# Performance work log

Measured on AMD Instinct MI355X. Metric: run time of the kernel, lower is better.

## Reference

```python
import jax, jax.numpy as jnp
import numpy as np

B, S, D, H = 4, 2048, 512, 8
DH = D // H  # head dim = 64
NEG = -1000000.0


def setup_inputs() -> dict:
    key = jax.random.key(0)
    ks = jax.random.split(key, 13)
    s = 1.0 / np.sqrt(D)
    return {
        "Q": jax.random.normal(ks[0], (B, S, D), jnp.float32),
        "K": jax.random.normal(ks[1], (B, S, D), jnp.float32),
        "V": jax.random.normal(ks[2], (B, S, D), jnp.float32),
        "Wq": jax.random.normal(ks[3], (D, D), jnp.float32) * s,
        "bq": jnp.zeros((D,), jnp.float32),
        "Wk": jax.random.normal(ks[4], (D, D), jnp.float32) * s,
        "bk": jnp.zeros((D,), jnp.float32),
        "Wv": jax.random.normal(ks[5], (D, D), jnp.float32) * s,
        "bv": jnp.zeros((D,), jnp.float32),
        "Wo": jax.random.normal(ks[6], (D, D), jnp.float32) * s,
        "bo": jnp.zeros((D,), jnp.float32),
        "masked": jax.random.randint(ks[7], (B,), 1, S + 1, jnp.int64),
    }


def _heads(x):
    # [B,S,D] -> [B,H,S,DH]
    return x.reshape(B, S, H, DH).transpose(0, 2, 1, 3)


def reference(Q, K, V, Wq, bq, Wk, bk, Wv, bv, Wo, bo, masked):
    q = _heads(Q @ Wq.T + bq)
    k = _heads(K @ Wk.T + bk)
    v = _heads(V @ Wv.T + bv)
    scores = jnp.einsum("bhqd,bhkd->bhqk", q, k) / jnp.sqrt(jnp.asarray(DH, q.dtype))
    # valid-length key mask, per batch (same for every head and query row)
    key_mask = jnp.arange(S)[None, None, None, :] < masked[:, None, None, None]
    scores = jnp.where(key_mask, scores, jnp.asarray(NEG, scores.dtype))
    weights = jax.nn.softmax(scores, axis=-1)
    out = jnp.einsum("bhqk,bhkd->bhqd", weights, v)  # [B,H,S,DH]
    out = out.transpose(0, 2, 1, 3).reshape(B, S, D)
    return out @ Wo.T + bo
```

## Files before the change

kernel.cpp:

```cpp
#include <hip/hip_runtime.h>
#include <stdint.h>


typedef __attribute__((ext_vector_type(8))) short short8;
typedef __attribute__((ext_vector_type(4))) float f32x4;
typedef __attribute__((ext_vector_type(4))) unsigned short u16x4;

#define MFMA16(a, b, c) __builtin_amdgcn_mfma_f32_16x16x32_bf16(a, b, c, 0, 0, 0)

#define SCALE_LOG2 0.18033688011112042f
#define FIXED_M    32.0f
#define MASKED_E2  -200.0f

__device__ __forceinline__ unsigned short f2bf(float f) {
    unsigned int x = __float_as_uint(f);
    unsigned int r = (x + 0x7fffu + ((x >> 16) & 1u)) >> 16;
    return (unsigned short)r;
}
__device__ __forceinline__ short8 load8(const unsigned short* p) {
    return *reinterpret_cast<const short8*>(p);
}
__device__ __forceinline__ void gload_lds16(const unsigned short* g, unsigned short* l) {
    __builtin_amdgcn_global_load_lds(
        (const __attribute__((address_space(1))) unsigned int*)g,
        (__attribute__((address_space(3))) unsigned int*)l, 16, 0, 0);
}

__global__ __launch_bounds__(256)
void convert_bf16(const float4* __restrict__ Q, const float4* __restrict__ K,
                  const float4* __restrict__ V, const float4* __restrict__ Wq,
                  const float4* __restrict__ Wk, const float4* __restrict__ Wv,
                  const float4* __restrict__ Wo, u16x4* __restrict__ dst)
{
    const int n = 3407872;
    for (int i = blockIdx.x * 256 + threadIdx.x; i < n; i += gridDim.x * 256) {
        const float4* src; int off;
        if      (i < 1048576) { src = Q;  off = i; }
        else if (i < 2097152) { src = K;  off = i - 1048576; }
        else if (i < 3145728) { src = V;  off = i - 2097152; }
        else if (i < 3211264) { src = Wq; off = i - 3145728; }
        else if (i < 3276800) { src = Wk; off = i - 3211264; }
        else if (i < 3342336) { src = Wv; off = i - 3276800; }
        else                  { src = Wo; off = i - 3342336; }
        const float4 v = src[off];
        u16x4 r;
        r[0] = f2bf(v.x); r[1] = f2bf(v.y); r[2] = f2bf(v.z); r[3] = f2bf(v.w);
        dst[i] = r;
    }
}

__global__ __launch_bounds__(256)
void gemm_bf(const unsigned short* __restrict__ Aall,
             const unsigned short* __restrict__ Wall,
             const float* __restrict__ b0, const float* __restrict__ b1,
             const float* __restrict__ b2,
             void* __restrict__ outall, int out_mode)
{
    __shared__ unsigned short As[128 * 64];
    __shared__ unsigned short Bs[128 * 64];

    const int z = blockIdx.y;
    const unsigned short* A = Aall + (long)z * 4194304;
    const unsigned short* W = Wall + z * 262144;
    const float* bias = (z == 0) ? b0 : (z == 1) ? b1 : b2;
    void* out = (out_mode == 0)
        ? (void*)((unsigned short*)outall + (long)z * 4194304) : outall;

    const int f    = blockIdx.x;
    const int xcd  = f & 7;
    const int slot = f >> 3;
    const int col0 = (slot & 3) * 128;
    const int row0 = ((slot >> 2) * 8 + xcd) * 128;

    const int tid  = threadIdx.x;
    const int lane = tid & 63;
    const int w    = tid >> 6;
    const int quad = lane >> 4;
    const int nlow = lane & 15;
    const int wm   = w >> 1, wn = w & 1;

    const unsigned short* ag[4];
    const unsigned short* wg[4];
    unsigned short *la[4], *lb[4];
#pragma unroll
    for (int i = 0; i < 4; i++) {
        const int s = i * 256 + tid;
        const int r = s >> 3, kcl = s & 7;
        const int kg = kcl ^ (r & 7);
        ag[i] = A + (long)(row0 + r) * 512 + kg * 8;
        wg[i] = W + (long)(col0 + r) * 512 + kg * 8;
        const int ldso = i * 2048 + ((tid >> 6) << 9);
        la[i] = As + ldso;
        lb[i] = Bs + ldso;
    }

    f32x4 acc[4][4];
#pragma unroll
    for (int t = 0; t < 4; t++)
#pragma unroll
        for (int g = 0; g < 4; g++) acc[t][g] = (f32x4){0.f, 0.f, 0.f, 0.f};

    for (int k0 = 0; k0 < 512; k0 += 64) {
#pragma unroll
        for (int i = 0; i < 4; i++) {
            gload_lds16(ag[i] + k0, la[i]);
            gload_lds16(wg[i] + k0, lb[i]);
        }
        __syncthreads();

        short8 af[4][2], bf[4][2];
#pragma unroll
        for (int t = 0; t < 4; t++) {
            const int rowa = wm * 64 + t * 16 + nlow;
            const int rowb = wn * 64 + t * 16 + nlow;
#pragma unroll
            for (int kc = 0; kc < 2; kc++) {
                const int c = (kc * 4 + quad) ^ (nlow & 7);
                af[t][kc] = load8(&As[(rowa * 8 + c) * 8]);
                bf[t][kc] = load8(&Bs[(rowb * 8 + c) * 8]);
            }
        }
#pragma unroll
        for (int kc = 0; kc < 2; kc++)
#pragma unroll
            for (int t = 0; t < 4; t++)
#pragma unroll
                for (int g = 0; g < 4; g++)
                    acc[t][g] = MFMA16(af[t][kc], bf[g][kc], acc[t][g]);
        __syncthreads();
    }

#pragma unroll
    for (int g = 0; g < 4; g++) {
        const int j = col0 + wn * 64 + g * 16 + nlow;
        const float bj = bias[j];
#pragma unroll
        for (int t = 0; t < 4; t++) {
#pragma unroll
            for (int r = 0; r < 4; r++) {
                const int i = row0 + wm * 64 + t * 16 + quad * 4 + r;
                const float v = acc[t][g][r] + bj;
                if (out_mode == 0) {
                    const int b = i >> 11, s = i & 2047;
                    const int h = j >> 6, dh = j & 63;
                    ((unsigned short*)out)[(((b * 8 + h) * 2048) + s) * 64 + dh] = f2bf(v);
                } else {
                    ((float*)out)[(long)i * 512 + j] = v;
                }
            }
        }
    }
}

__device__ __forceinline__ int ks_idx(int key, int dchunk) {
    return key * 64 + ((dchunk ^ (key & 7)) << 3);
}
__device__ __forceinline__ int vt_idx(int key, int dh) {
    return dh * 64 + ((((key >> 3) ^ (dh & 7) ^ ((dh >> 3) & 7)) << 3) + (key & 7));
}
__device__ __forceinline__ int ps_idx(int q, int key) {
    return q * 64 + ((((key >> 3) ^ (q & 7)) << 3) + (key & 7));
}

__global__ __launch_bounds__(256, 4)
void attn_kernel(const unsigned short* __restrict__ qp,
                 const unsigned short* __restrict__ kp,
                 const unsigned short* __restrict__ vp,
                 const void* __restrict__ masked,
                 unsigned short* __restrict__ out)
{
    __shared__ unsigned short Ks[2][4096];
    __shared__ unsigned short Vt[2][4096];
    __shared__ unsigned short Ps[4][1024];

    const int tid  = threadIdx.x;
    const int lane = tid & 63;
    const int w    = tid >> 6;
    const int quad = lane >> 4;
    const int nlow = lane & 15;

    const int f  = blockIdx.x;
    const int h  = f & 7;
    const int qb = (f >> 3) & 31;
    const int b  = f >> 8;
    const int q0 = qb * 64 + w * 16;
    const long base = ((long)(b * 8 + h)) * 2048 * 64;

    const long long first = *reinterpret_cast<const long long*>(masked);
    int kmax;
    if ((first >> 32) != 0) kmax = reinterpret_cast<const int*>(masked)[b];
    else                    kmax = (int)reinterpret_cast<const long long*>(masked)[b];
    kmax = min(max(kmax, 1), 2048);
    const int nkt = (kmax + 63) >> 6;

    const unsigned short* qrow = qp + base + (long)(q0 + nlow) * 64;
    const short8 aq0 = load8(qrow + quad * 8);
    const short8 aq1 = load8(qrow + 32 + quad * 8);

    short8 ones;
#pragma unroll
    for (int j = 0; j < 8; j++) ones[j] = (short)0x3F80;

    f32x4 o_acc[4], lacc;
#pragma unroll
    for (int vb = 0; vb < 4; vb++) o_acc[vb] = (f32x4){0.f, 0.f, 0.f, 0.f};
    lacc = (f32x4){0.f, 0.f, 0.f, 0.f};

    const int kr0 = tid >> 3;
    const int kr1 = 32 + kr0;
    const unsigned short* kg0 = kp + base + (long)kr0 * 64 + (((tid & 7) ^ (kr0 & 7)) << 3);
    const unsigned short* kg1 = kp + base + (long)kr1 * 64 + (((tid & 7) ^ (kr1 & 7)) << 3);
    const int kd0 = (w << 9);
    const int kd1 = 2048 + (w << 9);
    const int vk0 = tid >> 3;
    const int vk1 = 32 + vk0;
    const int vd0 = (tid & 7) << 3;
    const unsigned short* vg0 = vp + base + (long)vk0 * 64 + vd0;
    const unsigned short* vg1 = vp + base + (long)vk1 * 64 + vd0;

    gload_lds16(kg0, &Ks[0][kd0]);
    gload_lds16(kg1, &Ks[0][kd1]);
    {
        short8 v0 = load8(vg0);
        short8 v1 = load8(vg1);
#pragma unroll
        for (int j = 0; j < 8; j++) {
            Vt[0][vt_idx(vk0, vd0 + j)] = (unsigned short)v0[j];
            Vt[0][vt_idx(vk1, vd0 + j)] = (unsigned short)v1[j];
        }
    }
    __syncthreads();

    unsigned short* Psw = Ps[w];
    int cur = 0;
    short8 vv0, vv1;

    for (int kt = 0; kt < nkt; kt++) {
        const int k0 = kt * 64;
        const bool more = (kt + 1 < nkt);
        if (more) {
            const long off = (long)(k0 + 64) * 64;
            gload_lds16(kg0 + off, &Ks[cur ^ 1][kd0]);
            gload_lds16(kg1 + off, &Ks[cur ^ 1][kd1]);
            vv0 = load8(vg0 + off);
            vv1 = load8(vg1 + off);
        }
        const unsigned short* Ksc = Ks[cur];
        const unsigned short* Vtc = Vt[cur];

        f32x4 sacc[4];
#pragma unroll
        for (int kb = 0; kb < 4; kb++) sacc[kb] = (f32x4){0.f, 0.f, 0.f, 0.f};
#pragma unroll
        for (int kb = 0; kb < 4; kb++) {
            const int key = kb * 16 + nlow;
            short8 bk0 = load8(Ksc + ks_idx(key, quad));
            short8 bk1 = load8(Ksc + ks_idx(key, 4 + quad));
            sacc[kb] = MFMA16(aq0, bk0, sacc[kb]);
            sacc[kb] = MFMA16(aq1, bk1, sacc[kb]);
        }

#pragma unroll
        for (int kb = 0; kb < 4; kb++) {
            const bool valid = (k0 + kb * 16 + nlow) < kmax;
#pragma unroll
            for (int r = 0; r < 4; r++) {
                const int q = quad * 4 + r;
                const float e = valid ? fmaf(sacc[kb][r], SCALE_LOG2, -FIXED_M)
                                      : MASKED_E2;
                Psw[ps_idx(q, kb * 16 + nlow)] = f2bf(exp2f(e));
            }
        }
        __threadfence_block();

#pragma unroll
        for (int h2 = 0; h2 < 2; h2++) {
            const int g = h2 * 4 + quad;
            short8 ap = load8(Psw + ps_idx(nlow, g << 3));
            lacc = MFMA16(ap, ones, lacc);
#pragma unroll
            for (int vb = 0; vb < 4; vb++) {
                short8 bv = load8(Vtc + vt_idx(g << 3, vb * 16 + nlow));
                o_acc[vb] = MFMA16(ap, bv, o_acc[vb]);
            }
        }

        if (more) {
            unsigned short* Vtn = Vt[cur ^ 1];
#pragma unroll
            for (int j = 0; j < 8; j++) {
                Vtn[vt_idx(vk0, vd0 + j)] = (unsigned short)vv0[j];
                Vtn[vt_idx(vk1, vd0 + j)] = (unsigned short)vv1[j];
            }
        }
        __syncthreads();
        cur ^= 1;
    }

    float inv_l[4];
#pragma unroll
    for (int r = 0; r < 4; r++) inv_l[r] = 1.0f / lacc[r];
#pragma unroll
    for (int vb = 0; vb < 4; vb++) {
#pragma unroll
        for (int r = 0; r < 4; r++) {
            const int s   = q0 + quad * 4 + r;
            const int col = h * 64 + vb * 16 + nlow;
            out[(long)(b * 2048 + s) * 512 + col] = f2bf(o_acc[vb][r] * inv_l[r]);
        }
    }
}

extern "C" void kernel_launch(void* const* d_in, const int* in_sizes, int n_in,
                              void* d_out, int out_size, void* d_ws, size_t ws_size,
                              hipStream_t stream)
{
    const float4* Q  = (const float4*)d_in[0];
    const float4* K  = (const float4*)d_in[1];
    const float4* V  = (const float4*)d_in[2];
    const float4* Wq = (const float4*)d_in[3];
    const float*  bq = (const float*)d_in[4];
    const float4* Wk = (const float4*)d_in[5];
    const float*  bk = (const float*)d_in[6];
    const float4* Wv = (const float4*)d_in[7];
    const float*  bv = (const float*)d_in[8];
    const float4* Wo = (const float4*)d_in[9];
    const float*  bo = (const float*)d_in[10];
    const void*   masked = d_in[11];

    unsigned short* ws16 = (unsigned short*)d_ws;
    unsigned short* QKVb = ws16;
    unsigned short* Wb   = ws16 + 12582912;
    unsigned short* qp   = ws16 + 13631488;
    unsigned short* kp   = qp + 4194304;
    unsigned short* vp   = kp + 4194304;
    unsigned short* ao   = ws16;

    convert_bf16<<<2048, 256, 0, stream>>>(Q, K, V, Wq, Wk, Wv, Wo, (u16x4*)ws16);
    gemm_bf<<<dim3(256, 3), 256, 0, stream>>>(QKVb, Wb, bq, bk, bv, qp, 0);
    attn_kernel<<<dim3(1024), 256, 0, stream>>>(qp, kp, vp, masked, ao);
    gemm_bf<<<dim3(256, 1), 256, 0, stream>>>(ao, Wb + 3 * 262144, bo, bo, bo,
                                              d_out, 1);
}
```

Baseline: 176.2 us.

## Fuse fp32-to-bf16 conversion into projection GEMMs with double-buffered LDS

Removes the separate conversion kernel: the QKV and output projection GEMMs now read fp32 inputs and weights directly, convert them in registers with packed bf16 conversion instructions, and write them to swizzled shared memory. Shared memory is double-buffered so global loads for the next K tile are issued while the current tile's MFMAs run. This avoids a full write and reread of bf16 copies of Q, K, V and the weights. In exchange, each block reads twice the bytes (fp32), spends more registers on staged data, and the weights are converted repeatedly per block.

```diff
diff --git a/kernel.cpp b/kernel.cpp
--- a/kernel.cpp
+++ b/kernel.cpp
@@ -4,7 +4,6 @@
 
 typedef __attribute__((ext_vector_type(8))) short short8;
 typedef __attribute__((ext_vector_type(4))) float f32x4;
-typedef __attribute__((ext_vector_type(4))) unsigned short u16x4;
 
 #define MFMA16(a, b, c) __builtin_amdgcn_mfma_f32_16x16x32_bf16(a, b, c, 0, 0, 0)
 
@@ -17,54 +16,48 @@
     unsigned int r = (x + 0x7fffu + ((x >> 16) & 1u)) >> 16;
     return (unsigned short)r;
 }
+__device__ __forceinline__ unsigned int cvt_pk_bf16(float lo, float hi) {
+    unsigned int r;
+    asm("v_cvt_pk_bf16_f32 %0, %1, %2" : "=v"(r) : "v"(lo), "v"(hi));
+    return r;
+}
 __device__ __forceinline__ short8 load8(const unsigned short* p) {
     return *reinterpret_cast<const short8*>(p);
+}
+__device__ __forceinline__ float4 ld4(const float* p) {
+    return *reinterpret_cast<const float4*>(p);
 }
 __device__ __forceinline__ void gload_lds16(const unsigned short* g, unsigned short* l) {
     __builtin_amdgcn_global_load_lds(
         (const __attribute__((address_space(1))) unsigned int*)g,
         (__attribute__((address_space(3))) unsigned int*)l, 16, 0, 0);
 }
+__device__ __forceinline__ void cvt_write8(unsigned short* dst, float4 v0, float4 v1) {
+    uint4 d;
+    d.x = cvt_pk_bf16(v0.x, v0.y);
+    d.y = cvt_pk_bf16(v0.z, v0.w);
+    d.z = cvt_pk_bf16(v1.x, v1.y);
+    d.w = cvt_pk_bf16(v1.z, v1.w);
+    *reinterpret_cast<uint4*>(dst) = d;
+}
 
 __global__ __launch_bounds__(256)
-void convert_bf16(const float4* __restrict__ Q, const float4* __restrict__ K,
-                  const float4* __restrict__ V, const float4* __restrict__ Wq,
-                  const float4* __restrict__ Wk, const float4* __restrict__ Wv,
-                  const float4* __restrict__ Wo, u16x4* __restrict__ dst)
+void gemm_qkv(const float* __restrict__ Aq, const float* __restrict__ Ak,
+              const float* __restrict__ Av,
+              const float* __restrict__ Wqf, const float* __restrict__ Wkf,
+              const float* __restrict__ Wvf,
+              const float* __restrict__ bq, const float* __restrict__ bk,
+              const float* __restrict__ bv,
+              unsigned short* __restrict__ outall)
 {
-    const int n = 3407872;
-    for (int i = blockIdx.x * 256 + threadIdx.x; i < n; i += gridDim.x * 256) {
-        const float4* src; int off;
-        if      (i < 1048576) { src = Q;  off = i; }
-        else if (i < 2097152) { src = K;  off = i - 1048576; }
-        else if (i < 3145728) { src = V;  off = i - 2097152; }
-        else if (i < 3211264) { src = Wq; off = i - 3145728; }
-        else if (i < 3276800) { src = Wk; off = i - 3211264; }
-        else if (i < 3342336) { src = Wv; off = i - 3276800; }
-        else                  { src = Wo; off = i - 3342336; }
-        const float4 v = src[off];
-        u16x4 r;
-        r[0] = f2bf(v.x); r[1] = f2bf(v.y); r[2] = f2bf(v.z); r[3] = f2bf(v.w);
-        dst[i] = r;
-    }
-}
-
-__global__ __launch_bounds__(256)
-void gemm_bf(const unsigned short* __restrict__ Aall,
-             const unsigned short* __restrict__ Wall,
-             const float* __restrict__ b0, const float* __restrict__ b1,
-             const float* __restrict__ b2,
-             void* __restrict__ outall, int out_mode)
-{
-    __shared__ unsigned short As[128 * 64];
-    __shared__ unsigned short Bs[128 * 64];
+    __shared__ unsigned short As[2][8192];
+    __shared__ unsigned short Bs[2][8192];
 
     const int z = blockIdx.y;
-    const unsigned short* A = Aall + (long)z * 4194304;
-    const unsigned short* W = Wall + z * 262144;
-    const float* bias = (z == 0) ? b0 : (z == 1) ? b1 : b2;
-    void* out = (out_mode == 0)
-        ? (void*)((unsigned short*)outall + (long)z * 4194304) : outall;
+    const float* A    = (z == 0) ? Aq  : (z == 1) ? Ak  : Av;
+    const float* W    = (z == 0) ? Wqf : (z == 1) ? Wkf : Wvf;
+    const float* bias = (z == 0) ? bq  : (z == 1) ? bk  : bv;
+    unsigned short* out = outall + (long)z * 4194304;
 
     const int f    = blockIdx.x;
     const int xcd  = f & 7;
@@ -79,19 +72,17 @@
     const int nlow = lane & 15;
     const int wm   = w >> 1, wn = w & 1;
 
-    const unsigned short* ag[4];
-    const unsigned short* wg[4];
-    unsigned short *la[4], *lb[4];
+    const float* ag[4];
+    const float* wg[4];
+    int sw[4];
 #pragma unroll
     for (int i = 0; i < 4; i++) {
         const int s = i * 256 + tid;
-        const int r = s >> 3, kcl = s & 7;
-        const int kg = kcl ^ (r & 7);
+        const int r = s >> 3;
+        const int kg = (s & 7) ^ (r & 7);
         ag[i] = A + (long)(row0 + r) * 512 + kg * 8;
         wg[i] = W + (long)(col0 + r) * 512 + kg * 8;
-        const int ldso = i * 2048 + ((tid >> 6) << 9);
-        la[i] = As + ldso;
-        lb[i] = Bs + ldso;
+        sw[i] = s * 8;
     }
 
     f32x4 acc[4][4];
@@ -100,53 +91,175 @@
 #pragma unroll
         for (int g = 0; g < 4; g++) acc[t][g] = (f32x4){0.f, 0.f, 0.f, 0.f};
 
-    for (int k0 = 0; k0 < 512; k0 += 64) {
-#pragma unroll
-        for (int i = 0; i < 4; i++) {
-            gload_lds16(ag[i] + k0, la[i]);
-            gload_lds16(wg[i] + k0, lb[i]);
+    float4 ra[4][2], rw[4][2];
+#pragma unroll
+    for (int i = 0; i < 4; i++) {
+        ra[i][0] = ld4(ag[i]);     ra[i][1] = ld4(ag[i] + 4);
+        rw[i][0] = ld4(wg[i]);     rw[i][1] = ld4(wg[i] + 4);
+    }
+#pragma unroll
+    for (int i = 0; i < 4; i++) {
+        cvt_write8(&As[0][sw[i]], ra[i][0], ra[i][1]);
+        cvt_write8(&Bs[0][sw[i]], rw[i][0], rw[i][1]);
+    }
+    __syncthreads();
+
+    int cur = 0;
+    for (int k0 = 64; k0 <= 512; k0 += 64) {
+        const bool more = (k0 < 512);
+        if (more) {
+#pragma unroll
+            for (int i = 0; i < 4; i++) {
+                ra[i][0] = ld4(ag[i] + k0);     ra[i][1] = ld4(ag[i] + k0 + 4);
+                rw[i][0] = ld4(wg[i] + k0);     rw[i][1] = ld4(wg[i] + k0 + 4);
+            }
+        }
+#pragma unroll
+        for (int kc = 0; kc < 2; kc++) {
+            short8 af[4], bfr[4];
+#pragma unroll
+            for (int t = 0; t < 4; t++) {
+                const int rowa = wm * 64 + t * 16 + nlow;
+                const int rowb = wn * 64 + t * 16 + nlow;
+                const int ca = (kc * 4 + quad) ^ (nlow & 7);
+                af[t]  = load8(&As[cur][(rowa * 8 + ca) * 8]);
+                bfr[t] = load8(&Bs[cur][(rowb * 8 + ca) * 8]);
+            }
+#pragma unroll
+            for (int t = 0; t < 4; t++)
+#pragma unroll
+                for (int g = 0; g < 4; g++)
+                    acc[t][g] = MFMA16(af[t], bfr[g], acc[t][g]);
+        }
+        if (more) {
+#pragma unroll
+            for (int i = 0; i < 4; i++) {
+                cvt_write8(&As[cur ^ 1][sw[i]], ra[i][0], ra[i][1]);
+                cvt_write8(&Bs[cur ^ 1][sw[i]], rw[i][0], rw[i][1]);
+            }
         }
         __syncthreads();
-
-        short8 af[4][2], bf[4][2];
-#pragma unroll
-        for (int t = 0; t < 4; t++) {
-            const int rowa = wm * 64 + t * 16 + nlow;
-            const int rowb = wn * 64 + t * 16 + nlow;
-#pragma unroll
-            for (int kc = 0; kc < 2; kc++) {
-                const int c = (kc * 4 + quad) ^ (nlow & 7);
-                af[t][kc] = load8(&As[(rowa * 8 + c) * 8]);
-                bf[t][kc] = load8(&Bs[(rowb * 8 + c) * 8]);
-            }
-        }
-#pragma unroll
-        for (int kc = 0; kc < 2; kc++)
-#pragma unroll
-            for (int t = 0; t < 4; t++)
-#pragma unroll
-                for (int g = 0; g < 4; g++)
-                    acc[t][g] = MFMA16(af[t][kc], bf[g][kc], acc[t][g]);
-        __syncthreads();
+        cur ^= 1;
     }
 
 #pragma unroll
     for (int g = 0; g < 4; g++) {
         const int j = col0 + wn * 64 + g * 16 + nlow;
         const float bj = bias[j];
+        const int h = j >> 6, dh = j & 63;
 #pragma unroll
         for (int t = 0; t < 4; t++) {
 #pragma unroll
             for (int r = 0; r < 4; r++) {
                 const int i = row0 + wm * 64 + t * 16 + quad * 4 + r;
-                const float v = acc[t][g][r] + bj;
-                if (out_mode == 0) {
-                    const int b = i >> 11, s = i & 2047;
-                    const int h = j >> 6, dh = j & 63;
-                    ((unsigned short*)out)[(((b * 8 + h) * 2048) + s) * 64 + dh] = f2bf(v);
-                } else {
-                    ((float*)out)[(long)i * 512 + j] = v;
-                }
+                const int b = i >> 11, s = i & 2047;
+                out[(((b * 8 + h) * 2048) + s) * 64 + dh] = f2bf(acc[t][g][r] + bj);
+            }
+        }
+    }
+}
+
+__global__ __launch_bounds__(256)
+void gemm_out(const unsigned short* __restrict__ Aao,
+              const float* __restrict__ Wof, const float* __restrict__ bo,
+              float* __restrict__ outp)
+{
+    __shared__ unsigned short As[2][8192];
+    __shared__ unsigned short Bs[2][8192];
+
+    const int f    = blockIdx.x;
+    const int xcd  = f & 7;
+    const int slot = f >> 3;
+    const int col0 = (slot & 3) * 128;
+    const int row0 = ((slot >> 2) * 8 + xcd) * 128;
+
+    const int tid  = threadIdx.x;
+    const int lane = tid & 63;
+    const int w    = tid >> 6;
+    const int quad = lane >> 4;
+    const int nlow = lane & 15;
+    const int wm   = w >> 1, wn = w & 1;
+
+    const unsigned short* ag[4];
+    unsigned short* la[2][4];
+    const float* wg[4];
+    int sw[4];
+#pragma unroll
+    for (int i = 0; i < 4; i++) {
+        const int s = i * 256 + tid;
+        const int r = s >> 3;
+        const int kg = (s & 7) ^ (r & 7);
+        ag[i] = Aao + (long)(row0 + r) * 512 + kg * 8;
+        wg[i] = Wof + (long)(col0 + r) * 512 + kg * 8;
+        const int ldso = i * 2048 + (w << 9);
+        la[0][i] = &As[0][ldso];
+        la[1][i] = &As[1][ldso];
+        sw[i] = s * 8;
+    }
+
+    f32x4 acc[4][4];
+#pragma unroll
+    for (int t = 0; t < 4; t++)
+#pragma unroll
+        for (int g = 0; g < 4; g++) acc[t][g] = (f32x4){0.f, 0.f, 0.f, 0.f};
+
+    float4 rw[4][2];
+#pragma unroll
+    for (int i = 0; i < 4; i++) {
+        gload_lds16(ag[i], la[0][i]);
+        rw[i][0] = ld4(wg[i]);  rw[i][1] = ld4(wg[i] + 4);
+    }
+#pragma unroll
+    for (int i = 0; i < 4; i++)
+        cvt_write8(&Bs[0][sw[i]], rw[i][0], rw[i][1]);
+    __syncthreads();
+
+    int cur = 0;
+    for (int k0 = 64; k0 <= 512; k0 += 64) {
+        const bool more = (k0 < 512);
+        if (more) {
+#pragma unroll
+            for (int i = 0; i < 4; i++) {
+                gload_lds16(ag[i] + k0, la[cur ^ 1][i]);
+                rw[i][0] = ld4(wg[i] + k0);  rw[i][1] = ld4(wg[i] + k0 + 4);
+            }
+        }
+#pragma unroll
+        for (int kc = 0; kc < 2; kc++) {
+            short8 af[4], bfr[4];
+#pragma unroll
+            for (int t = 0; t < 4; t++) {
+                const int rowa = wm * 64 + t * 16 + nlow;
+                const int rowb = wn * 64 + t * 16 + nlow;
+                const int ca = (kc * 4 + quad) ^ (nlow & 7);
+                af[t]  = load8(&As[cur][(rowa * 8 + ca) * 8]);
+                bfr[t] = load8(&Bs[cur][(rowb * 8 + ca) * 8]);
+            }
+#pragma unroll
+            for (int t = 0; t < 4; t++)
+#pragma unroll
+                for (int g = 0; g < 4; g++)
+                    acc[t][g] = MFMA16(af[t], bfr[g], acc[t][g]);
+        }
+        if (more) {
+#pragma unroll
+            for (int i = 0; i < 4; i++)
+                cvt_write8(&Bs[cur ^ 1][sw[i]], rw[i][0], rw[i][1]);
+        }
+        __syncthreads();
+        cur ^= 1;
+    }
+
+#pragma unroll
+    for (int g = 0; g < 4; g++) {
+        const int j = col0 + wn * 64 + g * 16 + nlow;
+        const float bj = bo[j];
+#pragma unroll
+        for (int t = 0; t < 4; t++) {
+#pragma unroll
+            for (int r = 0; r < 4; r++) {
+                const int i = row0 + wm * 64 + t * 16 + quad * 4 + r;
+                outp[(long)i * 512 + j] = acc[t][g][r] + bj;
             }
         }
     }
@@ -315,30 +428,26 @@
                               void* d_out, int out_size, void* d_ws, size_t ws_size,
                               hipStream_t stream)
 {
-    const float4* Q  = (const float4*)d_in[0];
-    const float4* K  = (const float4*)d_in[1];
-    const float4* V  = (const float4*)d_in[2];
-    const float4* Wq = (const float4*)d_in[3];
-    const float*  bq = (const float*)d_in[4];
-    const float4* Wk = (const float4*)d_in[5];
-    const float*  bk = (const float*)d_in[6];
-    const float4* Wv = (const float4*)d_in[7];
-    const float*  bv = (const float*)d_in[8];
-    const float4* Wo = (const float4*)d_in[9];
-    const float*  bo = (const float*)d_in[10];
-    const void*   masked = d_in[11];
+    const float* Q  = (const float*)d_in[0];
+    const float* K  = (const float*)d_in[1];
+    const float* V  = (const float*)d_in[2];
+    const float* Wq = (const float*)d_in[3];
+    const float* bq = (const float*)d_in[4];
+    const float* Wk = (const float*)d_in[5];
+    const float* bk = (const float*)d_in[6];
+    const float* Wv = (const float*)d_in[7];
+    const float* bv = (const float*)d_in[8];
+    const float* Wo = (const float*)d_in[9];
+    const float* bo = (const float*)d_in[10];
+    const void*  masked = d_in[11];
 
     unsigned short* ws16 = (unsigned short*)d_ws;
-    unsigned short* QKVb = ws16;
-    unsigned short* Wb   = ws16 + 12582912;
-    unsigned short* qp   = ws16 + 13631488;
-    unsigned short* kp   = qp + 4194304;
-    unsigned short* vp   = kp + 4194304;
-    unsigned short* ao   = ws16;
-
-    convert_bf16<<<2048, 256, 0, stream>>>(Q, K, V, Wq, Wk, Wv, Wo, (u16x4*)ws16);
-    gemm_bf<<<dim3(256, 3), 256, 0, stream>>>(QKVb, Wb, bq, bk, bv, qp, 0);
+    unsigned short* qp = ws16;
+    unsigned short* kp = qp + 4194304;
+    unsigned short* vp = kp + 4194304;
+    unsigned short* ao = vp + 4194304;
+
+    gemm_qkv<<<dim3(256, 3), 256, 0, stream>>>(Q, K, V, Wq, Wk, Wv, bq, bk, bv, qp);
     attn_kernel<<<dim3(1024), 256, 0, stream>>>(qp, kp, vp, masked, ao);
-    gemm_bf<<<dim3(256, 1), 256, 0, stream>>>(ao, Wb + 3 * 262144, bo, bo, bo,
-                                              d_out, 1);
-}
+    gemm_out<<<dim3(256), 256, 0, stream>>>(ao, Wo, bo, (float*)d_out);
+}
```

New measurement: 182.6 us. 1.04x slower.

## Process two 16-row query groups per wave to reuse K/V tiles in attention

Applied to the files above, without the earlier changes.

Each wave now handles 32 query rows (two 16-row groups) instead of 16, so every block covers 128 queries and the grid is halved to 512 blocks. The K and V fragments loaded from LDS are reused across both query groups, halving K/V tile traffic per query and amortizing the global-to-LDS staging. s_setprio is added around the MFMA sections to favor matrix issue. The cost is more registers (occupancy hint lowered to 2), doubled P scratch in LDS, and fewer blocks, which can hurt load balance given the variable per-batch key lengths.

```diff
diff --git a/kernel.cpp b/kernel.cpp
--- a/kernel.cpp
+++ b/kernel.cpp
@@ -162,7 +162,7 @@
     return q * 64 + ((((key >> 3) ^ (q & 7)) << 3) + (key & 7));
 }
 
-__global__ __launch_bounds__(256, 4)
+__global__ __launch_bounds__(256, 2)
 void attn_kernel(const unsigned short* __restrict__ qp,
                  const unsigned short* __restrict__ kp,
                  const unsigned short* __restrict__ vp,
@@ -171,7 +171,7 @@
 {
     __shared__ unsigned short Ks[2][4096];
     __shared__ unsigned short Vt[2][4096];
-    __shared__ unsigned short Ps[4][1024];
+    __shared__ unsigned short Ps[4][2048];
 
     const int tid  = threadIdx.x;
     const int lane = tid & 63;
@@ -181,9 +181,9 @@
 
     const int f  = blockIdx.x;
     const int h  = f & 7;
-    const int qb = (f >> 3) & 31;
-    const int b  = f >> 8;
-    const int q0 = qb * 64 + w * 16;
+    const int qb = (f >> 3) & 15;
+    const int b  = f >> 7;
+    const int q0 = qb * 128 + w * 32;
     const long base = ((long)(b * 8 + h)) * 2048 * 64;
 
     const long long first = *reinterpret_cast<const long long*>(masked);
@@ -193,18 +193,25 @@
     kmax = min(max(kmax, 1), 2048);
     const int nkt = (kmax + 63) >> 6;
 
-    const unsigned short* qrow = qp + base + (long)(q0 + nlow) * 64;
-    const short8 aq0 = load8(qrow + quad * 8);
-    const short8 aq1 = load8(qrow + 32 + quad * 8);
+    short8 aq[2][2];
+#pragma unroll
+    for (int qg = 0; qg < 2; qg++) {
+        const unsigned short* qrow = qp + base + (long)(q0 + qg * 16 + nlow) * 64;
+        aq[qg][0] = load8(qrow + quad * 8);
+        aq[qg][1] = load8(qrow + 32 + quad * 8);
+    }
 
     short8 ones;
 #pragma unroll
     for (int j = 0; j < 8; j++) ones[j] = (short)0x3F80;
 
-    f32x4 o_acc[4], lacc;
-#pragma unroll
-    for (int vb = 0; vb < 4; vb++) o_acc[vb] = (f32x4){0.f, 0.f, 0.f, 0.f};
-    lacc = (f32x4){0.f, 0.f, 0.f, 0.f};
+    f32x4 o_acc[2][4], lacc[2];
+#pragma unroll
+    for (int qg = 0; qg < 2; qg++) {
+#pragma unroll
+        for (int vb = 0; vb < 4; vb++) o_acc[qg][vb] = (f32x4){0.f, 0.f, 0.f, 0.f};
+        lacc[qg] = (f32x4){0.f, 0.f, 0.f, 0.f};
+    }
 
     const int kr0 = tid >> 3;
     const int kr1 = 32 + kr0;
@@ -248,42 +255,60 @@
         const unsigned short* Ksc = Ks[cur];
         const unsigned short* Vtc = Vt[cur];
 
-        f32x4 sacc[4];
-#pragma unroll
-        for (int kb = 0; kb < 4; kb++) sacc[kb] = (f32x4){0.f, 0.f, 0.f, 0.f};
+        f32x4 sacc[2][4];
+#pragma unroll
+        for (int qg = 0; qg < 2; qg++)
+#pragma unroll
+            for (int kb = 0; kb < 4; kb++) sacc[qg][kb] = (f32x4){0.f, 0.f, 0.f, 0.f};
+        __builtin_amdgcn_s_setprio(1);
 #pragma unroll
         for (int kb = 0; kb < 4; kb++) {
             const int key = kb * 16 + nlow;
             short8 bk0 = load8(Ksc + ks_idx(key, quad));
             short8 bk1 = load8(Ksc + ks_idx(key, 4 + quad));
-            sacc[kb] = MFMA16(aq0, bk0, sacc[kb]);
-            sacc[kb] = MFMA16(aq1, bk1, sacc[kb]);
-        }
-
-#pragma unroll
-        for (int kb = 0; kb < 4; kb++) {
-            const bool valid = (k0 + kb * 16 + nlow) < kmax;
-#pragma unroll
-            for (int r = 0; r < 4; r++) {
-                const int q = quad * 4 + r;
-                const float e = valid ? fmaf(sacc[kb][r], SCALE_LOG2, -FIXED_M)
-                                      : MASKED_E2;
-                Psw[ps_idx(q, kb * 16 + nlow)] = f2bf(exp2f(e));
+#pragma unroll
+            for (int qg = 0; qg < 2; qg++) {
+                sacc[qg][kb] = MFMA16(aq[qg][0], bk0, sacc[qg][kb]);
+                sacc[qg][kb] = MFMA16(aq[qg][1], bk1, sacc[qg][kb]);
+            }
+        }
+        __builtin_amdgcn_s_setprio(0);
+
+#pragma unroll
+        for (int qg = 0; qg < 2; qg++) {
+            const int pb = qg << 10;
+#pragma unroll
+            for (int kb = 0; kb < 4; kb++) {
+                const bool valid = (k0 + kb * 16 + nlow) < kmax;
+#pragma unroll
+                for (int r = 0; r < 4; r++) {
+                    const int q = quad * 4 + r;
+                    const float e = valid ? fmaf(sacc[qg][kb][r], SCALE_LOG2, -FIXED_M)
+                                          : MASKED_E2;
+                    Psw[pb + ps_idx(q, kb * 16 + nlow)] = f2bf(exp2f(e));
+                }
             }
         }
         __threadfence_block();
 
+        __builtin_amdgcn_s_setprio(1);
 #pragma unroll
         for (int h2 = 0; h2 < 2; h2++) {
             const int g = h2 * 4 + quad;
-            short8 ap = load8(Psw + ps_idx(nlow, g << 3));
-            lacc = MFMA16(ap, ones, lacc);
-#pragma unroll
-            for (int vb = 0; vb < 4; vb++) {
-                short8 bv = load8(Vtc + vt_idx(g << 3, vb * 16 + nlow));
-                o_acc[vb] = MFMA16(ap, bv, o_acc[vb]);
-            }
-        }
+            short8 bv[4];
+#pragma unroll
+            for (int vb = 0; vb < 4; vb++)
+                bv[vb] = load8(Vtc + vt_idx(g << 3, vb * 16 + nlow));
+#pragma unroll
+            for (int qg = 0; qg < 2; qg++) {
+                short8 ap = load8(&Psw[(qg << 10) + ps_idx(nlow, g << 3)]);
+                lacc[qg] = MFMA16(ap, ones, lacc[qg]);
+#pragma unroll
+                for (int vb = 0; vb < 4; vb++)
+                    o_acc[qg][vb] = MFMA16(ap, bv[vb], o_acc[qg][vb]);
+            }
+        }
+        __builtin_amdgcn_s_setprio(0);
 
         if (more) {
             unsigned short* Vtn = Vt[cur ^ 1];
@@ -297,16 +322,19 @@
         cur ^= 1;
     }
 
-    float inv_l[4];
-#pragma unroll
-    for (int r = 0; r < 4; r++) inv_l[r] = 1.0f / lacc[r];
-#pragma unroll
-    for (int vb = 0; vb < 4; vb++) {
-#pragma unroll
-        for (int r = 0; r < 4; r++) {
-            const int s   = q0 + quad * 4 + r;
-            const int col = h * 64 + vb * 16 + nlow;
-            out[(long)(b * 2048 + s) * 512 + col] = f2bf(o_acc[vb][r] * inv_l[r]);
+#pragma unroll
+    for (int qg = 0; qg < 2; qg++) {
+        float inv_l[4];
+#pragma unroll
+        for (int r = 0; r < 4; r++) inv_l[r] = 1.0f / lacc[qg][r];
+#pragma unroll
+        for (int vb = 0; vb < 4; vb++) {
+#pragma unroll
+            for (int r = 0; r < 4; r++) {
+                const int s   = q0 + qg * 16 + quad * 4 + r;
+                const int col = h * 64 + vb * 16 + nlow;
+                out[(long)(b * 2048 + s) * 512 + col] = f2bf(o_acc[qg][vb][r] * inv_l[r]);
+            }
         }
     }
 }
@@ -338,7 +366,7 @@
 
     convert_bf16<<<2048, 256, 0, stream>>>(Q, K, V, Wq, Wk, Wv, Wo, (u16x4*)ws16);
     gemm_bf<<<dim3(256, 3), 256, 0, stream>>>(QKVb, Wb, bq, bk, bv, qp, 0);
-    attn_kernel<<<dim3(1024), 256, 0, stream>>>(qp, kp, vp, masked, ao);
+    attn_kernel<<<dim3(512), 256, 0, stream>>>(qp, kp, vp, masked, ao);
     gemm_bf<<<dim3(256, 1), 256, 0, stream>>>(ao, Wb + 3 * 262144, bo, bo, bo,
                                               d_out, 1);
 }
```

Result: slower. 190.0 us (+7.9%).
